# Kernel tuning notes

Hardware: AMD Instinct MI355X
Metric: run time of the kernel (lower is better)

Reference implementation:

```python
import jax, jax.numpy as jnp
import numpy as np

H = 768        # hidden_size (rubert-base)
WDIM = 30      # width_embedding_dim (SpanRepresentation default)
MAXW = 10      # max_span_width
HID = 150      # PairwiseScorer hidden_dim
LN_EPS = 1e-5


def setup_inputs() -> dict:
    key = jax.random.key(0)
    ks = jax.random.split(key, 12)
    B, S, N = 4, 2048, 4096
    p = lambda i, shape: jax.random.normal(ks[i], shape, dtype=jnp.float32) * 0.02
    return {
        "sequence_output": jax.random.normal(ks[0], (B, S, H), dtype=jnp.float32),
        "span_starts": jax.random.randint(ks[1], (B, N), 0, S),
        "span_ends": jax.random.randint(ks[2], (B, N), 0, S),
        "W_start": p(3, (H, H)), "b_start": jnp.zeros((H,), jnp.float32),
        "W_end": p(4, (H, H)), "b_end": jnp.zeros((H,), jnp.float32),
        "width_emb": p(5, (MAXW + 1, WDIM)),
        "W_out": p(6, (2 * H + WDIM, H)), "b_out": jnp.zeros((H,), jnp.float32),
        "w_ment": p(7, (H,)), "b_ment": jnp.zeros((), jnp.float32),
        "W1": p(8, (4 * H, HID)), "b1": jnp.zeros((HID,), jnp.float32),
        "ln_g": jnp.ones((HID,), jnp.float32), "ln_b": jnp.zeros((HID,), jnp.float32),
        "W2": p(9, (HID,)), "b2": jnp.zeros((), jnp.float32),
        "top_k": 128,
    }


def reference(sequence_output, span_starts, span_ends,
              W_start, b_start, W_end, b_end, width_emb, W_out, b_out,
              w_ment, b_ment, W1, b1, ln_g, ln_b, W2, b2, top_k):
    # --- SpanRepresentation: gather endpoints, endpoint FFs, width embedding ---
    st = jnp.take_along_axis(sequence_output, span_starts[..., None], axis=1)  # [B,N,H]
    en = jnp.take_along_axis(sequence_output, span_ends[..., None], axis=1)    # [B,N,H]
    start_e = st @ W_start + b_start
    end_e = en @ W_end + b_end
    widths = jnp.clip(span_ends - span_starts, 0, MAXW)
    we = width_emb[widths]                                                     # [B,N,WDIM]
    span_repr = jnp.concatenate([start_e, end_e, we], axis=-1) @ W_out + b_out # [B,N,H]

    # --- MentionScorer + top-k filtering (per batch, vectorized) ---
    scores = span_repr @ w_ment + b_ment                                       # [B,N]
    mention_scores, idx = jax.lax.top_k(scores, top_k)                         # [B,K]
    repr_k = jnp.take_along_axis(span_repr, idx[..., None], axis=1)            # [B,K,H]
    f_starts = jnp.take_along_axis(span_starts, idx, axis=1)
    f_ends = jnp.take_along_axis(span_ends, idx, axis=1)

    # --- PairwiseScorer over all pairs: cat([s1,s2,s1-s2,s1*s2]) @ W1 ---
    # Split W1 rows into the four feature blocks; fold the (s1-s2) block in:
    #   z = s1@(Wa+Wc) + s2@(Wb-Wc) + (s1*s2)@Wd + b1
    Wa, Wb, Wc, Wd = W1[:H], W1[H:2*H], W1[2*H:3*H], W1[3*H:]
    u = repr_k @ (Wa + Wc)                                                     # [B,K,HID]
    v = repr_k @ (Wb - Wc)                                                     # [B,K,HID]
    pw = jnp.einsum('bih,bjh,hd->bijd', repr_k, repr_k, Wd)                    # [B,K,K,HID]
    z = u[:, :, None, :] + v[:, None, :, :] + pw + b1
    h = jax.nn.relu(z)
    mu = jnp.mean(h, axis=-1, keepdims=True)
    var = jnp.mean(jnp.square(h - mu), axis=-1, keepdims=True)
    hn = (h - mu) * jax.lax.rsqrt(var + LN_EPS) * ln_g + ln_b
    # Dropout(0.3) is identity in eval mode.
    ant = hn @ W2 + b2                                                         # [B,K,K]
    ant = jnp.tril(ant, k=-1)

    return (mention_scores, ant, f_starts, f_ends)
```

## Files before the change

kernel.cpp:

```cpp
#include <hip/hip_runtime.h>
#include <math.h>

#define H 768
#define SEQ 2048
#define NSP 4096
#define HIDD 150
#define TOPK 128
#define NPAD 160

#define OFS_ANT 512
#define OFS_FS 66048
#define OFS_FE 66560

static const size_t OFF_T     = 0ull;
static const size_t OFF_BIASP = 8448ull;
static const size_t OFF_WOV   = 14592ull;
static const size_t OFF_AV    = 16128ull;
static const size_t OFF_CV    = 16896ull;
static const size_t OFF_TW    = 17664ull;
static const size_t OFF_PD    = 17680ull;
static const size_t OFF_CAND  = 34064ull;
static const size_t OFF_FS    = 42256ull;
static const size_t OFF_FE    = 42768ull;
static const size_t OFF_WID   = 43280ull;
static const size_t OFF_UVP   = 43792ull;
static const size_t OFF_GW    = 371472ull;
static const size_t OFF_SCAL  = 371632ull;
static const size_t OFF_WF    = 371640ull;
static const size_t OFF_WCF   = 433080ull;
static const size_t OFF_RJF   = 555960ull;
static const size_t OFF_RKH   = 752568ull;
static const size_t OFF_SE    = 949176ull;
static const size_t OFF_SEP   = 1735608ull;

typedef __attribute__((ext_vector_type(8))) _Float16 half8;
typedef __attribute__((ext_vector_type(4))) float f32x4;

__global__ __launch_bounds__(256) void kA(
    const float* __restrict__ b_start, const float* __restrict__ b_end,
    const float* __restrict__ b_out, const float* __restrict__ W_out,
    const float* __restrict__ w_ment, const float* __restrict__ W1,
    const float* __restrict__ ln_g, const float* __restrict__ ln_b,
    const float* __restrict__ W2, const float* __restrict__ b2,
    float* __restrict__ biasP, float* __restrict__ WOV,
    _Float16* __restrict__ WF, _Float16* __restrict__ WCF,
    float* __restrict__ GW, float* __restrict__ SCAL) {
    const int blk = blockIdx.x, tid = threadIdx.x;
    if (blk < 24) {
        const int kc = blk / 3, jb = blk - kc * 3;
        const int j = jb * 256 + tid;
        float acc = (kc == 0) ? b_out[j] : 0.f;
        const int k0 = kc * 96;
#pragma unroll 4
        for (int k = k0; k < k0 + 96; ++k) {
            acc += b_start[k] * W_out[(size_t)k * H + j];
            acc += b_end[k]   * W_out[(size_t)(H + k) * H + j];
        }
        biasP[kc * H + j] = acc;
    } else if (blk < 408) {
        const int wid = tid >> 6, lane = tid & 63;
        const int gr = (blk - 24) * 4 + wid;
        const float* row = W_out + (size_t)gr * H;
        float s = 0.f;
#pragma unroll
        for (int q = 0; q < 12; ++q) s += row[lane + 64 * q] * w_ment[lane + 64 * q];
#pragma unroll
        for (int off = 32; off; off >>= 1) s += __shfl_down(s, off, 64);
        if (lane == 0) WOV[gr] = s;
    } else if (blk < 468) {
        const int idx = (blk - 408) * 256 + tid;
        const int nt = idx / 1536;
        const int rem = idx - nt * 1536;
        const int kt = rem >> 6, lane = rem & 63;
        const int n = nt * 16 + (lane & 15);
        const int kb = kt * 32 + (lane >> 4) * 8;
        _Float16* dst = WF + (size_t)idx * 8;
#pragma unroll
        for (int e = 0; e < 8; ++e) {
            float v = (n < HIDD) ? W1[(size_t)(3 * H + kb + e) * HIDD + n] : 0.f;
            dst[e] = (_Float16)v;
        }
    } else if (blk < 588) {
        const int idx = (blk - 468) * 256 + tid;
        const int nt = idx / 1536;
        const int rem = idx - nt * 1536;
        const int kt = rem >> 6, lane = rem & 63;
        const int n = nt * 16 + (lane & 15);
        const int kb = kt * 32 + (lane >> 4) * 8;
        _Float16* dst = WCF + (size_t)idx * 8;
#pragma unroll
        for (int e = 0; e < 8; ++e) {
            const int h = kb + e;
            float v = 0.f;
            if (n < 160) {
                if (n < HIDD)
                    v = W1[(size_t)h * HIDD + n] + W1[(size_t)(2 * H + h) * HIDD + n];
            } else {
                const int d = n - 160;
                if (d < HIDD)
                    v = W1[(size_t)(H + h) * HIDD + d] - W1[(size_t)(2 * H + h) * HIDD + d];
            }
            dst[e] = (_Float16)v;
        }
    } else {
        if (tid < NPAD) GW[tid] = (tid < HIDD) ? ln_g[tid] * W2[tid] : 0.f;
        if (tid == 0) {
            float sg = 0.f, sb = 0.f;
            for (int d = 0; d < HIDD; ++d) { sg += ln_g[d] * W2[d]; sb += ln_b[d] * W2[d]; }
            SCAL[0] = sg;
            SCAL[1] = sb + b2[0];
        }
    }
}

__global__ __launch_bounds__(256) void kB(
    const float* __restrict__ biasP, const float* __restrict__ width_emb,
    const float* __restrict__ W_out, const float* __restrict__ W_start,
    const float* __restrict__ W_end, const float* __restrict__ WOV,
    float* __restrict__ T, float* __restrict__ av, float* __restrict__ cv) {
    const int blk = blockIdx.x, tid = threadIdx.x;
    if (blk < 33) {
        const int w = blk / 3, jb = blk - w * 3;
        const int j = jb * 256 + tid;
        float acc = 0.f;
#pragma unroll
        for (int kc = 0; kc < 8; ++kc) acc += biasP[kc * H + j];
#pragma unroll
        for (int k = 0; k < 30; ++k)
            acc += width_emb[w * 30 + k] * W_out[(size_t)(2 * H + k) * H + j];
        T[w * H + j] = acc;
    } else {
        const int wid = tid >> 6, lane = tid & 63;
        const int gr = (blk - 33) * 4 + wid;
        const float* row = (gr < H) ? (W_start + (size_t)gr * H) : (W_end + (size_t)(gr - H) * H);
        const float* vec = (gr < H) ? WOV : (WOV + H);
        float s = 0.f;
#pragma unroll
        for (int q = 0; q < 12; ++q) s += row[lane + 64 * q] * vec[lane + 64 * q];
#pragma unroll
        for (int off = 32; off; off >>= 1) s += __shfl_down(s, off, 64);
        if (lane == 0) {
            if (gr < H) av[gr] = s; else cv[gr - H] = s;
        }
    }
}

__global__ void k_posdots(const float* __restrict__ seq, const float* __restrict__ av,
                          const float* __restrict__ cv, const float* __restrict__ T,
                          const float* __restrict__ w_ment, const float* __restrict__ b_ment,
                          float* __restrict__ PD, float* __restrict__ tw) {
    const int wid = threadIdx.x >> 6, lane = threadIdx.x & 63;
    if (blockIdx.x < 2048) {
        const int r = blockIdx.x * 4 + wid;
        const float4* row = (const float4*)(seq + (size_t)r * H);
        const float4* a4 = (const float4*)av;
        const float4* c4 = (const float4*)cv;
        float sa = 0.f, sc = 0.f;
#pragma unroll
        for (int q = 0; q < 3; ++q) {
            float4 x = row[lane + 64 * q];
            float4 ya = a4[lane + 64 * q], yc = c4[lane + 64 * q];
            sa += x.x * ya.x + x.y * ya.y + x.z * ya.z + x.w * ya.w;
            sc += x.x * yc.x + x.y * yc.y + x.z * yc.z + x.w * yc.w;
        }
#pragma unroll
        for (int off = 32; off; off >>= 1) {
            sa += __shfl_down(sa, off, 64);
            sc += __shfl_down(sc, off, 64);
        }
        if (lane == 0) { PD[r] = sa; PD[8192 + r] = sc; }
    } else {
        for (int w = wid; w <= 10; w += 4) {
            float s = 0.f;
#pragma unroll
            for (int q = 0; q < 12; ++q) s += T[w * H + lane + 64 * q] * w_ment[lane + 64 * q];
#pragma unroll
            for (int off = 32; off; off >>= 1) s += __shfl_down(s, off, 64);
            if (lane == 0) tw[w] = s + b_ment[0];
        }
    }
}

__global__ __launch_bounds__(256) void k_sort1(const float* __restrict__ PD,
    const int* __restrict__ starts, const int* __restrict__ ends,
    const float* __restrict__ tw, unsigned long long* __restrict__ CAND) {
    __shared__ unsigned long long keys[512];
    const int blk = blockIdx.x;
    const int b = blk >> 3, c = blk & 7;
    const int tid = threadIdx.x;
    for (int i = tid; i < 512; i += 256) {
        const int gi = c * 512 + i;
        const int r = b * NSP + gi;
        const int s = starts[r], e = ends[r];
        int w = e - s; w = w < 0 ? 0 : (w > 10 ? 10 : w);
        const float sc = PD[b * SEQ + s] + PD[8192 + b * SEQ + e] + tw[w];
        unsigned u = __float_as_uint(sc);
        u = (u & 0x80000000u) ? ~u : (u | 0x80000000u);
        keys[i] = ((unsigned long long)u << 32) | (unsigned)(0xFFFFFFFFu - (unsigned)gi);
    }
    __syncthreads();
    for (int k = 2; k <= 512; k <<= 1) {
        for (int j = k >> 1; j > 0; j >>= 1) {
            const int p = tid;
            const int i = ((p & ~(j - 1)) << 1) | (p & (j - 1));
            const int l = i | j;
            unsigned long long a = keys[i], d = keys[l];
            const bool desc = ((i & k) == 0);
            if ((a < d) == desc) { keys[i] = d; keys[l] = a; }
            __syncthreads();
        }
    }
    if (tid < 128) CAND[(size_t)(b * 8 + c) * 128 + tid] = keys[tid];
}

__global__ __launch_bounds__(512) void k_sort2(const unsigned long long* __restrict__ CAND,
    const int* __restrict__ starts, const int* __restrict__ ends,
    float* __restrict__ out, int* __restrict__ fsI, int* __restrict__ feI,
    int* __restrict__ widI) {
    __shared__ unsigned long long keys[1024];
    const int b = blockIdx.x;
    const int tid = threadIdx.x;
    for (int i = tid; i < 1024; i += 512) keys[i] = CAND[(size_t)b * 1024 + i];
    __syncthreads();
    for (int k = 2; k <= 1024; k <<= 1) {
        for (int j = k >> 1; j > 0; j >>= 1) {
            const int p = tid;
            const int i = ((p & ~(j - 1)) << 1) | (p & (j - 1));
            const int l = i | j;
            unsigned long long a = keys[i], d = keys[l];
            const bool desc = ((i & k) == 0);
            if ((a < d) == desc) { keys[i] = d; keys[l] = a; }
            __syncthreads();
        }
    }
    if (tid < TOPK) {
        const unsigned long long key = keys[tid];
        const int widx = (int)(0xFFFFFFFFu - (unsigned)(key & 0xFFFFFFFFu));
        const unsigned hu = (unsigned)(key >> 32);
        const float sval = __uint_as_float((hu & 0x80000000u) ? (hu & 0x7FFFFFFFu) : ~hu);
        const int s = starts[b * NSP + widx], e = ends[b * NSP + widx];
        const int p = b * TOPK + tid;
        out[p] = sval;
        out[OFS_FS + p] = (float)s;
        out[OFS_FE + p] = (float)e;
        fsI[p] = b * SEQ + s;
        feI[p] = b * SEQ + e;
        int w = e - s;
        widI[p] = w < 0 ? 0 : (w > 10 ? 10 : w);
    }
}

__global__ __launch_bounds__(256) void k_se(const float* __restrict__ seq,
    const int* __restrict__ fsI, const int* __restrict__ feI,
    const float* __restrict__ W_start, const float* __restrict__ W_end,
    float* __restrict__ SEP) {
    __shared__ float sA[16][68];
    __shared__ float sB[16][68];
    __shared__ int sRow[64];
    const int tid = threadIdx.x;
    const int n0 = blockIdx.x * 64, m0 = blockIdx.y * 64, z = blockIdx.z;
    const int which = z >> 2;
    const int kbase = (z & 3) * 192;
    const int* rsrc = which ? feI : fsI;
    if (tid < 64) sRow[tid] = rsrc[m0 + tid];
    __syncthreads();
    const float* W = which ? W_end : W_start;
    const int tr = tid >> 4, tc = tid & 15;
    const int rr = tid >> 2, kg = (tid & 3) * 4;
    const int kb = tid >> 4, jc = (tid & 15) * 4;
    float acc[4][4];
#pragma unroll
    for (int i = 0; i < 4; ++i)
#pragma unroll
        for (int j = 0; j < 4; ++j) acc[i][j] = 0.f;
    for (int k0 = kbase; k0 < kbase + 192; k0 += 16) {
        float4 va = *(const float4*)(seq + (size_t)sRow[rr] * H + k0 + kg);
        float4 vb = *(const float4*)(W + (size_t)(k0 + kb) * H + n0 + jc);
        sA[kg + 0][rr] = va.x; sA[kg + 1][rr] = va.y;
        sA[kg + 2][rr] = va.z; sA[kg + 3][rr] = va.w;
        *(float4*)&sB[kb][jc] = vb;
        __syncthreads();
#pragma unroll
        for (int kk = 0; kk < 16; ++kk) {
            float a[4], b[4];
            *(float4*)a = *(const float4*)&sA[kk][tr * 4];
            *(float4*)b = *(const float4*)&sB[kk][tc * 4];
#pragma unroll
            for (int i = 0; i < 4; ++i)
#pragma unroll
                for (int j = 0; j < 4; ++j) acc[i][j] += a[i] * b[j];
        }
        __syncthreads();
    }
    float* dst = SEP + (size_t)z * 512 * H;
#pragma unroll
    for (int i = 0; i < 4; ++i) {
        float4 o = make_float4(acc[i][0], acc[i][1], acc[i][2], acc[i][3]);
        *(float4*)(dst + (size_t)(m0 + tr * 4 + i) * H + n0 + tc * 4) = o;
    }
}

__global__ void k_reduceSE(const float* __restrict__ SEP, float* __restrict__ SE) {
    const int p = blockIdx.x, tid = threadIdx.x;
    if (tid >= 192) return;
    const int which = p >> 9, row = p & 511;
    const int c0 = tid * 4;
    float4 s = make_float4(0.f, 0.f, 0.f, 0.f);
#pragma unroll
    for (int kc = 0; kc < 4; ++kc) {
        float4 v = *(const float4*)(SEP + ((size_t)((which << 2) | kc) * 512 + row) * H + c0);
        s.x += v.x; s.y += v.y; s.z += v.z; s.w += v.w;
    }
    *(float4*)(SE + (size_t)p * H + c0) = s;
}

__global__ __launch_bounds__(256) void k_rk(const float* __restrict__ SE,
    const float* __restrict__ W_out, float* __restrict__ RKP) {
    __shared__ float sA[16][68];
    __shared__ float sB[16][68];
    const int tid = threadIdx.x;
    const int n0 = blockIdx.x * 64, m0 = blockIdx.y * 64, z = blockIdx.z;
    const int ph = z >> 2;
    const int kbase = (z & 3) * 192;
    const float* A = SE + (size_t)ph * 512 * H;
    const float* B = W_out + (size_t)ph * H * H;
    const int tr = tid >> 4, tc = tid & 15;
    const int rr = tid >> 2, kg = (tid & 3) * 4;
    const int kb = tid >> 4, jc = (tid & 15) * 4;
    float acc[4][4];
#pragma unroll
    for (int i = 0; i < 4; ++i)
#pragma unroll
        for (int j = 0; j < 4; ++j) acc[i][j] = 0.f;
    for (int k0 = kbase; k0 < kbase + 192; k0 += 16) {
        float4 va = *(const float4*)(A + (size_t)(m0 + rr) * H + k0 + kg);
        float4 vb = *(const float4*)(B + (size_t)(k0 + kb) * H + n0 + jc);
        sA[kg + 0][rr] = va.x; sA[kg + 1][rr] = va.y;
        sA[kg + 2][rr] = va.z; sA[kg + 3][rr] = va.w;
        *(float4*)&sB[kb][jc] = vb;
        __syncthreads();
#pragma unroll
        for (int kk = 0; kk < 16; ++kk) {
            float a[4], b[4];
            *(float4*)a = *(const float4*)&sA[kk][tr * 4];
            *(float4*)b = *(const float4*)&sB[kk][tc * 4];
#pragma unroll
            for (int i = 0; i < 4; ++i)
#pragma unroll
                for (int j = 0; j < 4; ++j) acc[i][j] += a[i] * b[j];
        }
        __syncthreads();
    }
    float* dst = RKP + (size_t)z * 512 * H;
#pragma unroll
    for (int i = 0; i < 4; ++i) {
        float4 o = make_float4(acc[i][0], acc[i][1], acc[i][2], acc[i][3]);
        *(float4*)(dst + (size_t)(m0 + tr * 4 + i) * H + n0 + tc * 4) = o;
    }
}

__global__ __launch_bounds__(256) void k_reduce(const float* __restrict__ RKpart,
    const float* __restrict__ T, const int* __restrict__ widI,
    _Float16* __restrict__ RKH, _Float16* __restrict__ RJF) {
    __shared__ float srow[H];
    const int p = blockIdx.x, tid = threadIdx.x;
    const int w = widI[p];
    if (tid < 192) {
        const int c0 = tid * 4;
        float4 s = *(const float4*)(T + (size_t)w * H + c0);
#pragma unroll
        for (int kc = 0; kc < 8; ++kc) {
            float4 v = *(const float4*)(RKpart + ((size_t)kc * 512 + p) * H + c0);
            s.x += v.x; s.y += v.y; s.z += v.z; s.w += v.w;
        }
        *(float4*)&srow[c0] = s;
        _Float16* hd = RKH + (size_t)p * H + c0;
        hd[0] = (_Float16)s.x; hd[1] = (_Float16)s.y;
        hd[2] = (_Float16)s.z; hd[3] = (_Float16)s.w;
    }
    __syncthreads();
    if (tid < 96) {
        const int k0 = tid * 8;
        const int kt = k0 >> 5, sub = k0 & 31;
        const int lane = (p & 15) | ((sub >> 3) << 4);
        const int t = p >> 4;
        _Float16* d2 = RJF + ((size_t)(t * 24 + kt) * 64 + lane) * 8;
#pragma unroll
        for (int e = 0; e < 8; ++e) d2[e] = (_Float16)srow[k0 + e];
    }
}

__global__ __launch_bounds__(256) void k_uv3(const _Float16* __restrict__ RJF,
    const _Float16* __restrict__ WCF, float* __restrict__ UVP) {
    const int t = blockIdx.x, kh = blockIdx.y;
    const int wave = threadIdx.x >> 6, lane = threadIdx.x & 63;
    const _Float16* Af = RJF + (size_t)t * 24 * 64 * 8;
    f32x4 acc[5];
#pragma unroll
    for (int q = 0; q < 5; ++q) acc[q] = (f32x4){0.f, 0.f, 0.f, 0.f};
    for (int kk = 0; kk < 12; ++kk) {
        const int kt = kh * 12 + kk;
        half8 a = *(const half8*)(Af + ((size_t)(kt * 64 + lane)) * 8);
#pragma unroll
        for (int q = 0; q < 5; ++q) {
            const int nt = wave * 5 + q;
            half8 bv = *(const half8*)(WCF + ((size_t)((nt * 24 + kt) * 64 + lane)) * 8);
            acc[q] = __builtin_amdgcn_mfma_f32_16x16x32_f16(a, bv, acc[q], 0, 0, 0);
        }
    }
    const int c = lane & 15, g = lane >> 4;
#pragma unroll
    for (int q = 0; q < 5; ++q) {
        const int n = (wave * 5 + q) * 16 + c;
#pragma unroll
        for (int r = 0; r < 4; ++r) {
            const int p = t * 16 + g * 4 + r;
            UVP[((size_t)kh * 512 + p) * 320 + n] = acc[q][r];
        }
    }
}

__global__ __launch_bounds__(256) void k_pair(
    const _Float16* __restrict__ RJF, const _Float16* __restrict__ WF,
    const _Float16* __restrict__ RKH, const float* __restrict__ UVP,
    const float* __restrict__ b1, const float* __restrict__ GW,
    const float* __restrict__ SCAL, float* __restrict__ ant) {
    const int ii = blockIdx.x, b = blockIdx.y;
    float* arow = ant + ((size_t)b * TOPK + ii) * TOPK;
    const int tid = threadIdx.x;
    if (tid < TOPK && tid >= ii) arow[tid] = 0.f;
    const int ntiles = (ii + 15) >> 4;
    if (ntiles == 0) return;

    const int wave = tid >> 6, lane = tid & 63;
    const int g = lane >> 4, c = lane & 15;
    const int t0 = wave, t1 = wave + 4;
    const bool has0 = t0 < ntiles, has1 = t1 < ntiles;

    __shared__ _Float16 sB[2][5120];

    const _Float16* RiH = RKH + (size_t)(b * TOPK + ii) * H;
    const _Float16* Aj0 = RJF + (size_t)(b * 8 + t0) * 24 * 64 * 8;
    const _Float16* Aj1 = RJF + (size_t)(b * 8 + (t1 < 8 ? t1 : 7)) * 24 * 64 * 8;

    f32x4 acc0[10], acc1[10];
#pragma unroll
    for (int nt = 0; nt < 10; ++nt) {
        acc0[nt] = (f32x4){0.f, 0.f, 0.f, 0.f};
        acc1[nt] = (f32x4){0.f, 0.f, 0.f, 0.f};
    }

    auto stage_src = [&](int kt, int i) -> uint4 {
        const int nt = i >> 6, wi = i & 63;
        return *(const uint4*)(WF + ((size_t)((nt * 24 + kt) * 64 + wi)) * 8);
    };

    uint4 s0 = stage_src(0, tid);
    uint4 s1 = stage_src(0, tid + 256);
    uint4 s2;
    if (tid < 128) s2 = stage_src(0, tid + 512);
    {
        uint4* sbw = (uint4*)sB[0];
        sbw[tid] = s0;
        sbw[tid + 256] = s1;
        if (tid < 128) sbw[tid + 512] = s2;
    }
    half8 rj0, rj1, ri;
    if (has0) rj0 = *(const half8*)(Aj0 + (size_t)lane * 8);
    if (has1) rj1 = *(const half8*)(Aj1 + (size_t)lane * 8);
    ri = *(const half8*)(RiH + g * 8);
    __syncthreads();

    for (int kt = 0; kt < 24; ++kt) {
        const int cur = kt & 1, nxt = cur ^ 1;
        uint4 n0, n1, n2;
        half8 nrj0, nrj1, nri;
        if (kt < 23) {
            n0 = stage_src(kt + 1, tid);
            n1 = stage_src(kt + 1, tid + 256);
            if (tid < 128) n2 = stage_src(kt + 1, tid + 512);
            if (has0) nrj0 = *(const half8*)(Aj0 + ((size_t)((kt + 1) * 64 + lane)) * 8);
            if (has1) nrj1 = *(const half8*)(Aj1 + ((size_t)((kt + 1) * 64 + lane)) * 8);
            nri = *(const half8*)(RiH + (kt + 1) * 32 + g * 8);
        }
        half8 a0, a1;
        if (has0) a0 = ri * rj0;
        if (has1) a1 = ri * rj1;
#pragma unroll
        for (int nt = 0; nt < 10; ++nt) {
            half8 bv = *(const half8*)&sB[cur][nt * 512 + lane * 8];
            if (has0) acc0[nt] = __builtin_amdgcn_mfma_f32_16x16x32_f16(a0, bv, acc0[nt], 0, 0, 0);
            if (has1) acc1[nt] = __builtin_amdgcn_mfma_f32_16x16x32_f16(a1, bv, acc1[nt], 0, 0, 0);
        }
        if (kt < 23) {
            uint4* sbw = (uint4*)sB[nxt];
            sbw[tid] = n0;
            sbw[tid + 256] = n1;
            if (tid < 128) sbw[tid + 512] = n2;
            rj0 = nrj0; rj1 = nrj1; ri = nri;
        }
        __syncthreads();
    }

    const float Sgw = SCAL[0], C0 = SCAL[1];
    const int pi = b * TOPK + ii;
    float u10[10], gw10[10];
#pragma unroll
    for (int nt = 0; nt < 10; ++nt) {
        const int d = nt * 16 + c;
        const float ub = (d < HIDD) ? b1[d] : 0.f;
        u10[nt] = UVP[(size_t)pi * 320 + d] + UVP[(size_t)(512 + pi) * 320 + d] + ub;
        gw10[nt] = GW[d];
    }
    auto epi = [&](const f32x4 (&acc)[10], int t) {
#pragma unroll
        for (int r = 0; r < 4; ++r) {
            const int j = 16 * t + g * 4 + r;
            const int pj = b * TOPK + j;
            const float* Vp0 = UVP + (size_t)pj * 320 + 160;
            const float* Vp1 = UVP + (size_t)(512 + pj) * 320 + 160;
            float s1 = 0.f, s2 = 0.f, s3 = 0.f;
#pragma unroll
            for (int nt = 0; nt < 10; ++nt) {
                const int d = nt * 16 + c;
                float z = acc[nt][r] + u10[nt] + Vp0[d] + Vp1[d];
                float h = (d < HIDD && z > 0.f) ? z : 0.f;
                s1 += h;
                s2 += h * h;
                s3 += h * gw10[nt];
            }
#pragma unroll
            for (int off = 1; off < 16; off <<= 1) {
                s1 += __shfl_xor(s1, off, 64);
                s2 += __shfl_xor(s2, off, 64);
                s3 += __shfl_xor(s3, off, 64);
            }
            const float mu = s1 * (1.f / HIDD);
            const float var = s2 * (1.f / HIDD) - mu * mu;
            const float rstd = rsqrtf(var + 1e-5f);
            const float val = rstd * (s3 - mu * Sgw) + C0;
            if (c == 0 && j < ii) arow[j] = val;
        }
    };
    if (has0) epi(acc0, t0);
    if (has1) epi(acc1, t1);
}

extern "C" void kernel_launch(void* const* d_in, const int* in_sizes, int n_in,
                              void* d_out, int out_size, void* d_ws, size_t ws_size,
                              hipStream_t stream) {
    const float* seq      = (const float*)d_in[0];
    const int*   starts   = (const int*)d_in[1];
    const int*   ends     = (const int*)d_in[2];
    const float* W_start  = (const float*)d_in[3];
    const float* b_start  = (const float*)d_in[4];
    const float* W_end    = (const float*)d_in[5];
    const float* b_end    = (const float*)d_in[6];
    const float* width_e  = (const float*)d_in[7];
    const float* W_out    = (const float*)d_in[8];
    const float* b_out    = (const float*)d_in[9];
    const float* w_ment   = (const float*)d_in[10];
    const float* b_ment   = (const float*)d_in[11];
    const float* W1       = (const float*)d_in[12];
    const float* b1       = (const float*)d_in[13];
    const float* ln_g     = (const float*)d_in[14];
    const float* ln_b     = (const float*)d_in[15];
    const float* W2       = (const float*)d_in[16];
    const float* b2       = (const float*)d_in[17];
    float* out = (float*)d_out;
    float* ws  = (float*)d_ws;

    float* Tt    = ws + OFF_T;
    float* biasP = ws + OFF_BIASP;
    float* WOV   = ws + OFF_WOV;
    float* av    = ws + OFF_AV;
    float* cv    = ws + OFF_CV;
    float* tw    = ws + OFF_TW;
    float* PD    = ws + OFF_PD;
    unsigned long long* CANDp = (unsigned long long*)(ws + OFF_CAND);
    int*   fsI   = (int*)(ws + OFF_FS);
    int*   feI   = (int*)(ws + OFF_FE);
    int*   widI  = (int*)(ws + OFF_WID);
    float* UVPp  = ws + OFF_UVP;
    float* GWp   = ws + OFF_GW;
    float* SCALp = ws + OFF_SCAL;
    _Float16* WFp  = (_Float16*)(ws + OFF_WF);
    _Float16* WCFp = (_Float16*)(ws + OFF_WCF);
    _Float16* RJFp = (_Float16*)(ws + OFF_RJF);
    _Float16* RKHp = (_Float16*)(ws + OFF_RKH);
    float* SEp   = ws + OFF_SE;
    float* SEPp  = ws + OFF_SEP;

    kA<<<589, 256, 0, stream>>>(b_start, b_end, b_out, W_out, w_ment, W1,
                                ln_g, ln_b, W2, b2, biasP, WOV, WFp, WCFp, GWp, SCALp);
    kB<<<417, 256, 0, stream>>>(biasP, width_e, W_out, W_start, W_end, WOV, Tt, av, cv);
    k_posdots<<<2049, 256, 0, stream>>>(seq, av, cv, Tt, w_ment, b_ment, PD, tw);
    k_sort1<<<32, 256, 0, stream>>>(PD, starts, ends, tw, CANDp);
    k_sort2<<<4, 512, 0, stream>>>(CANDp, starts, ends, out, fsI, feI, widI);
    k_se<<<dim3(12, 8, 8), 256, 0, stream>>>(seq, fsI, feI, W_start, W_end, SEPp);
    k_reduceSE<<<1024, 192, 0, stream>>>(SEPp, SEp);
    k_rk<<<dim3(12, 8, 8), 256, 0, stream>>>(SEp, W_out, SEPp);
    k_reduce<<<512, 256, 0, stream>>>(SEPp, Tt, widI, RKHp, RJFp);
    k_uv3<<<dim3(32, 2), 256, 0, stream>>>(RJFp, WCFp, UVPp);
    k_pair<<<dim3(128, 4), 256, 0, stream>>>(RJFp, WFp, RKHp, UVPp, b1, GWp, SCALp,
                                             out + OFS_ANT);
}
```

Baseline: 237.5 us.

## Move top-k span projection GEMMs to fp16 MFMA and replace final bitonic sort with merge

```diff
diff --git a/kernel.cpp b/kernel.cpp
--- a/kernel.cpp
+++ b/kernel.cpp
@@ -28,12 +28,16 @@
 static const size_t OFF_SCAL  = 371632ull;
 static const size_t OFF_WF    = 371640ull;
 static const size_t OFF_WCF   = 433080ull;
-static const size_t OFF_RJF   = 555960ull;
-static const size_t OFF_RKH   = 752568ull;
-static const size_t OFF_SE    = 949176ull;
-static const size_t OFF_SEP   = 1735608ull;
+static const size_t OFF_WSF   = 555960ull;
+static const size_t OFF_WEF   = 850872ull;
+static const size_t OFF_WOF   = 1145784ull;
+static const size_t OFF_GSEH  = 1735608ull;
+static const size_t OFF_SEH   = 2128824ull;
+static const size_t OFF_RKH   = 2522040ull;
+static const size_t OFF_RKP2  = 2718648ull;
 
 typedef __attribute__((ext_vector_type(8))) _Float16 half8;
+typedef __attribute__((ext_vector_type(4))) _Float16 half4;
 typedef __attribute__((ext_vector_type(4))) float f32x4;
 
 __global__ __launch_bounds__(256) void kA(
@@ -42,9 +46,11 @@
     const float* __restrict__ w_ment, const float* __restrict__ W1,
     const float* __restrict__ ln_g, const float* __restrict__ ln_b,
     const float* __restrict__ W2, const float* __restrict__ b2,
+    const float* __restrict__ W_start, const float* __restrict__ W_end,
     float* __restrict__ biasP, float* __restrict__ WOV,
     _Float16* __restrict__ WF, _Float16* __restrict__ WCF,
-    float* __restrict__ GW, float* __restrict__ SCAL) {
+    _Float16* __restrict__ WSF, _Float16* __restrict__ WEF,
+    _Float16* __restrict__ WOF, float* __restrict__ GW, float* __restrict__ SCAL) {
     const int blk = blockIdx.x, tid = threadIdx.x;
     if (blk < 24) {
         const int kc = blk / 3, jb = blk - kc * 3;
@@ -102,7 +108,7 @@
             }
             dst[e] = (_Float16)v;
         }
-    } else {
+    } else if (blk == 588) {
         if (tid < NPAD) GW[tid] = (tid < HIDD) ? ln_g[tid] * W2[tid] : 0.f;
         if (tid == 0) {
             float sg = 0.f, sb = 0.f;
@@ -110,6 +116,29 @@
             SCAL[0] = sg;
             SCAL[1] = sb + b2[0];
         }
+    } else if (blk < 1165) {
+        const bool isS = blk < 877;
+        const int idx = (blk - (isS ? 589 : 877)) * 256 + tid;
+        const float* Wsrc = isS ? W_start : W_end;
+        _Float16* dstb = isS ? WSF : WEF;
+        const int nt = idx / 1536;
+        const int rem = idx - nt * 1536;
+        const int kt = rem >> 6, lane = rem & 63;
+        const int n = nt * 16 + (lane & 15);
+        const int kb = kt * 32 + (lane >> 4) * 8;
+        _Float16* dst = dstb + (size_t)idx * 8;
+#pragma unroll
+        for (int e = 0; e < 8; ++e) dst[e] = (_Float16)Wsrc[(size_t)(kb + e) * H + n];
+    } else {
+        const int idx = (blk - 1165) * 256 + tid;
+        const int nt = idx / 3072;
+        const int rem = idx - nt * 3072;
+        const int kt = rem >> 6, lane = rem & 63;
+        const int n = nt * 16 + (lane & 15);
+        const int kb = kt * 32 + (lane >> 4) * 8;
+        _Float16* dst = WOF + (size_t)idx * 8;
+#pragma unroll
+        for (int e = 0; e < 8; ++e) dst[e] = (_Float16)W_out[(size_t)(kb + e) * H + n];
     }
 }
 
@@ -213,28 +242,48 @@
     if (tid < 128) CAND[(size_t)(b * 8 + c) * 128 + tid] = keys[tid];
 }
 
-__global__ __launch_bounds__(512) void k_sort2(const unsigned long long* __restrict__ CAND,
+__global__ __launch_bounds__(256) void k_sort2(const unsigned long long* __restrict__ CAND,
     const int* __restrict__ starts, const int* __restrict__ ends,
     float* __restrict__ out, int* __restrict__ fsI, int* __restrict__ feI,
     int* __restrict__ widI) {
-    __shared__ unsigned long long keys[1024];
-    const int b = blockIdx.x;
-    const int tid = threadIdx.x;
-    for (int i = tid; i < 1024; i += 512) keys[i] = CAND[(size_t)b * 1024 + i];
+    __shared__ unsigned long long K[1024];
+    const int b = blockIdx.x, tid = threadIdx.x;
+    for (int i = tid; i < 1024; i += 256) K[i] = CAND[(size_t)b * 1024 + i];
     __syncthreads();
-    for (int k = 2; k <= 1024; k <<= 1) {
-        for (int j = k >> 1; j > 0; j >>= 1) {
-            const int p = tid;
-            const int i = ((p & ~(j - 1)) << 1) | (p & (j - 1));
-            const int l = i | j;
-            unsigned long long a = keys[i], d = keys[l];
-            const bool desc = ((i & k) == 0);
-            if ((a < d) == desc) { keys[i] = d; keys[l] = a; }
+    for (int nl = 4; nl >= 1; nl >>= 1) {
+        const int items = nl * 128;
+        unsigned long long v0 = 0, v1 = 0;
+        if (tid < items) {
+            const int q = tid >> 7, r = tid & 127;
+            unsigned long long a = K[q * 256 + r];
+            unsigned long long d = K[q * 256 + 128 + (127 - r)];
+            v0 = a > d ? a : d;
+        }
+        if (tid + 256 < items) {
+            const int i = tid + 256;
+            const int q = i >> 7, r = i & 127;
+            unsigned long long a = K[q * 256 + r];
+            unsigned long long d = K[q * 256 + 128 + (127 - r)];
+            v1 = a > d ? a : d;
+        }
+        __syncthreads();
+        if (tid < items) K[(tid >> 7) * 128 + (tid & 127)] = v0;
+        if (tid + 256 < items) { const int i = tid + 256; K[(i >> 7) * 128 + (i & 127)] = v1; }
+        __syncthreads();
+        for (int j = 64; j; j >>= 1) {
+            const int pairs = nl * 64;
+            for (int i = tid; i < pairs; i += 256) {
+                const int q = i >> 6, r = i & 63;
+                const int lo = q * 128 + (((r & ~(j - 1)) << 1) | (r & (j - 1)));
+                const int hi = lo + j;
+                unsigned long long a = K[lo], d = K[hi];
+                if (a < d) { K[lo] = d; K[hi] = a; }
+            }
             __syncthreads();
         }
     }
     if (tid < TOPK) {
-        const unsigned long long key = keys[tid];
+        const unsigned long long key = K[tid];
         const int widx = (int)(0xFFFFFFFFu - (unsigned)(key & 0xFFFFFFFFu));
         const unsigned hu = (unsigned)(key >> 32);
         const float sval = __uint_as_float((hu & 0x80000000u) ? (hu & 0x7FFFFFFFu) : ~hu);
@@ -250,157 +299,96 @@
     }
 }
 
-__global__ __launch_bounds__(256) void k_se(const float* __restrict__ seq,
-    const int* __restrict__ fsI, const int* __restrict__ feI,
-    const float* __restrict__ W_start, const float* __restrict__ W_end,
-    float* __restrict__ SEP) {
-    __shared__ float sA[16][68];
-    __shared__ float sB[16][68];
-    __shared__ int sRow[64];
+__global__ void k_gath(const float* __restrict__ seq, const int* __restrict__ fsI,
+                       const int* __restrict__ feI, _Float16* __restrict__ GSEH) {
+    const int r0 = blockIdx.x * 4;
     const int tid = threadIdx.x;
-    const int n0 = blockIdx.x * 64, m0 = blockIdx.y * 64, z = blockIdx.z;
-    const int which = z >> 2;
-    const int kbase = (z & 3) * 192;
-    const int* rsrc = which ? feI : fsI;
-    if (tid < 64) sRow[tid] = rsrc[m0 + tid];
-    __syncthreads();
-    const float* W = which ? W_end : W_start;
-    const int tr = tid >> 4, tc = tid & 15;
-    const int rr = tid >> 2, kg = (tid & 3) * 4;
-    const int kb = tid >> 4, jc = (tid & 15) * 4;
-    float acc[4][4];
-#pragma unroll
-    for (int i = 0; i < 4; ++i)
-#pragma unroll
-        for (int j = 0; j < 4; ++j) acc[i][j] = 0.f;
-    for (int k0 = kbase; k0 < kbase + 192; k0 += 16) {
-        float4 va = *(const float4*)(seq + (size_t)sRow[rr] * H + k0 + kg);
-        float4 vb = *(const float4*)(W + (size_t)(k0 + kb) * H + n0 + jc);
-        sA[kg + 0][rr] = va.x; sA[kg + 1][rr] = va.y;
-        sA[kg + 2][rr] = va.z; sA[kg + 3][rr] = va.w;
-        *(float4*)&sB[kb][jc] = vb;
-        __syncthreads();
-#pragma unroll
-        for (int kk = 0; kk < 16; ++kk) {
-            float a[4], b[4];
-            *(float4*)a = *(const float4*)&sA[kk][tr * 4];
-            *(float4*)b = *(const float4*)&sB[kk][tc * 4];
-#pragma unroll
-            for (int i = 0; i < 4; ++i)
-#pragma unroll
-                for (int j = 0; j < 4; ++j) acc[i][j] += a[i] * b[j];
-        }
-        __syncthreads();
-    }
-    float* dst = SEP + (size_t)z * 512 * H;
-#pragma unroll
-    for (int i = 0; i < 4; ++i) {
-        float4 o = make_float4(acc[i][0], acc[i][1], acc[i][2], acc[i][3]);
-        *(float4*)(dst + (size_t)(m0 + tr * 4 + i) * H + n0 + tc * 4) = o;
-    }
-}
-
-__global__ void k_reduceSE(const float* __restrict__ SEP, float* __restrict__ SE) {
+    for (int q = 0; q < 4; ++q) {
+        const int row = r0 + q;
+        const int src = (row < 512) ? fsI[row] : feI[row - 512];
+        if (tid < 192) {
+            float4 v = *(const float4*)(seq + (size_t)src * H + tid * 4);
+            half4 h = {(_Float16)v.x, (_Float16)v.y, (_Float16)v.z, (_Float16)v.w};
+            *(half4*)(GSEH + (size_t)row * H + tid * 4) = h;
+        }
+    }
+}
+
+__global__ __launch_bounds__(256) void k_gemm1(const _Float16* __restrict__ GSEH,
+    const _Float16* __restrict__ WSF, const _Float16* __restrict__ WEF,
+    _Float16* __restrict__ SEH) {
+    const int mt = blockIdx.x;
+    const int wave = threadIdx.x >> 6, lane = threadIdx.x & 63;
+    const int nt0 = blockIdx.y * 8 + wave * 2;
+    const _Float16* Arow = GSEH + (size_t)(mt * 16 + (lane & 15)) * H + (lane >> 4) * 8;
+    const _Float16* BF = (mt < 32) ? WSF : WEF;
+    f32x4 acc0 = {0.f, 0.f, 0.f, 0.f}, acc1 = acc0;
+    for (int kt = 0; kt < 24; ++kt) {
+        half8 a = *(const half8*)(Arow + kt * 32);
+        half8 b0 = *(const half8*)(BF + ((size_t)((nt0 * 24 + kt) * 64 + lane)) * 8);
+        half8 b1 = *(const half8*)(BF + ((size_t)(((nt0 + 1) * 24 + kt) * 64 + lane)) * 8);
+        acc0 = __builtin_amdgcn_mfma_f32_16x16x32_f16(a, b0, acc0, 0, 0, 0);
+        acc1 = __builtin_amdgcn_mfma_f32_16x16x32_f16(a, b1, acc1, 0, 0, 0);
+    }
+    const int c = lane & 15, quad = lane >> 4;
+#pragma unroll
+    for (int r = 0; r < 4; ++r) {
+        const int row = mt * 16 + quad * 4 + r;
+        SEH[(size_t)row * H + nt0 * 16 + c] = (_Float16)acc0[r];
+        SEH[(size_t)row * H + (nt0 + 1) * 16 + c] = (_Float16)acc1[r];
+    }
+}
+
+__global__ __launch_bounds__(256) void k_gemm2(const _Float16* __restrict__ SEH,
+    const _Float16* __restrict__ WOF, float* __restrict__ RKP2) {
+    const int mt = blockIdx.x, kh = blockIdx.z;
+    const int wave = threadIdx.x >> 6, lane = threadIdx.x & 63;
+    const int nt0 = blockIdx.y * 8 + wave * 2;
+    const _Float16* Arow = SEH + (size_t)(kh * 512 + mt * 16 + (lane & 15)) * H + (lane >> 4) * 8;
+    f32x4 acc0 = {0.f, 0.f, 0.f, 0.f}, acc1 = acc0;
+    for (int kt2 = 0; kt2 < 24; ++kt2) {
+        const int kt = kh * 24 + kt2;
+        half8 a = *(const half8*)(Arow + kt2 * 32);
+        half8 b0 = *(const half8*)(WOF + ((size_t)((nt0 * 48 + kt) * 64 + lane)) * 8);
+        half8 b1 = *(const half8*)(WOF + ((size_t)(((nt0 + 1) * 48 + kt) * 64 + lane)) * 8);
+        acc0 = __builtin_amdgcn_mfma_f32_16x16x32_f16(a, b0, acc0, 0, 0, 0);
+        acc1 = __builtin_amdgcn_mfma_f32_16x16x32_f16(a, b1, acc1, 0, 0, 0);
+    }
+    const int c = lane & 15, quad = lane >> 4;
+    float* dst = RKP2 + (size_t)kh * 512 * H;
+#pragma unroll
+    for (int r = 0; r < 4; ++r) {
+        const int row = mt * 16 + quad * 4 + r;
+        dst[(size_t)row * H + nt0 * 16 + c] = acc0[r];
+        dst[(size_t)row * H + (nt0 + 1) * 16 + c] = acc1[r];
+    }
+}
+
+__global__ void k_fin(const float* __restrict__ RKP2, const float* __restrict__ T,
+                      const int* __restrict__ widI, _Float16* __restrict__ RKH) {
     const int p = blockIdx.x, tid = threadIdx.x;
     if (tid >= 192) return;
-    const int which = p >> 9, row = p & 511;
+    const int w = widI[p];
     const int c0 = tid * 4;
-    float4 s = make_float4(0.f, 0.f, 0.f, 0.f);
-#pragma unroll
-    for (int kc = 0; kc < 4; ++kc) {
-        float4 v = *(const float4*)(SEP + ((size_t)((which << 2) | kc) * 512 + row) * H + c0);
-        s.x += v.x; s.y += v.y; s.z += v.z; s.w += v.w;
-    }
-    *(float4*)(SE + (size_t)p * H + c0) = s;
-}
-
-__global__ __launch_bounds__(256) void k_rk(const float* __restrict__ SE,
-    const float* __restrict__ W_out, float* __restrict__ RKP) {
-    __shared__ float sA[16][68];
-    __shared__ float sB[16][68];
-    const int tid = threadIdx.x;
-    const int n0 = blockIdx.x * 64, m0 = blockIdx.y * 64, z = blockIdx.z;
-    const int ph = z >> 2;
-    const int kbase = (z & 3) * 192;
-    const float* A = SE + (size_t)ph * 512 * H;
-    const float* B = W_out + (size_t)ph * H * H;
-    const int tr = tid >> 4, tc = tid & 15;
-    const int rr = tid >> 2, kg = (tid & 3) * 4;
-    const int kb = tid >> 4, jc = (tid & 15) * 4;
-    float acc[4][4];
-#pragma unroll
-    for (int i = 0; i < 4; ++i)
-#pragma unroll
-        for (int j = 0; j < 4; ++j) acc[i][j] = 0.f;
-    for (int k0 = kbase; k0 < kbase + 192; k0 += 16) {
-        float4 va = *(const float4*)(A + (size_t)(m0 + rr) * H + k0 + kg);
-        float4 vb = *(const float4*)(B + (size_t)(k0 + kb) * H + n0 + jc);
-        sA[kg + 0][rr] = va.x; sA[kg + 1][rr] = va.y;
-        sA[kg + 2][rr] = va.z; sA[kg + 3][rr] = va.w;
-        *(float4*)&sB[kb][jc] = vb;
-        __syncthreads();
-#pragma unroll
-        for (int kk = 0; kk < 16; ++kk) {
-            float a[4], b[4];
-            *(float4*)a = *(const float4*)&sA[kk][tr * 4];
-            *(float4*)b = *(const float4*)&sB[kk][tc * 4];
-#pragma unroll
-            for (int i = 0; i < 4; ++i)
-#pragma unroll
-                for (int j = 0; j < 4; ++j) acc[i][j] += a[i] * b[j];
-        }
-        __syncthreads();
-    }
-    float* dst = RKP + (size_t)z * 512 * H;
-#pragma unroll
-    for (int i = 0; i < 4; ++i) {
-        float4 o = make_float4(acc[i][0], acc[i][1], acc[i][2], acc[i][3]);
-        *(float4*)(dst + (size_t)(m0 + tr * 4 + i) * H + n0 + tc * 4) = o;
-    }
-}
-
-__global__ __launch_bounds__(256) void k_reduce(const float* __restrict__ RKpart,
-    const float* __restrict__ T, const int* __restrict__ widI,
-    _Float16* __restrict__ RKH, _Float16* __restrict__ RJF) {
-    __shared__ float srow[H];
-    const int p = blockIdx.x, tid = threadIdx.x;
-    const int w = widI[p];
-    if (tid < 192) {
-        const int c0 = tid * 4;
-        float4 s = *(const float4*)(T + (size_t)w * H + c0);
-#pragma unroll
-        for (int kc = 0; kc < 8; ++kc) {
-            float4 v = *(const float4*)(RKpart + ((size_t)kc * 512 + p) * H + c0);
-            s.x += v.x; s.y += v.y; s.z += v.z; s.w += v.w;
-        }
-        *(float4*)&srow[c0] = s;
-        _Float16* hd = RKH + (size_t)p * H + c0;
-        hd[0] = (_Float16)s.x; hd[1] = (_Float16)s.y;
-        hd[2] = (_Float16)s.z; hd[3] = (_Float16)s.w;
-    }
-    __syncthreads();
-    if (tid < 96) {
-        const int k0 = tid * 8;
-        const int kt = k0 >> 5, sub = k0 & 31;
-        const int lane = (p & 15) | ((sub >> 3) << 4);
-        const int t = p >> 4;
-        _Float16* d2 = RJF + ((size_t)(t * 24 + kt) * 64 + lane) * 8;
-#pragma unroll
-        for (int e = 0; e < 8; ++e) d2[e] = (_Float16)srow[k0 + e];
-    }
-}
-
-__global__ __launch_bounds__(256) void k_uv3(const _Float16* __restrict__ RJF,
+    float4 s = *(const float4*)(T + (size_t)w * H + c0);
+    float4 v0 = *(const float4*)(RKP2 + (size_t)p * H + c0);
+    float4 v1 = *(const float4*)(RKP2 + (size_t)(512 + p) * H + c0);
+    half4 h = {(_Float16)(s.x + v0.x + v1.x), (_Float16)(s.y + v0.y + v1.y),
+               (_Float16)(s.z + v0.z + v1.z), (_Float16)(s.w + v0.w + v1.w)};
+    *(half4*)(RKH + (size_t)p * H + c0) = h;
+}
+
+__global__ __launch_bounds__(256) void k_uv3(const _Float16* __restrict__ RKH,
     const _Float16* __restrict__ WCF, float* __restrict__ UVP) {
     const int t = blockIdx.x, kh = blockIdx.y;
     const int wave = threadIdx.x >> 6, lane = threadIdx.x & 63;
-    const _Float16* Af = RJF + (size_t)t * 24 * 64 * 8;
+    const _Float16* Arow = RKH + (size_t)(t * 16 + (lane & 15)) * H + (lane >> 4) * 8;
     f32x4 acc[5];
 #pragma unroll
     for (int q = 0; q < 5; ++q) acc[q] = (f32x4){0.f, 0.f, 0.f, 0.f};
     for (int kk = 0; kk < 12; ++kk) {
         const int kt = kh * 12 + kk;
-        half8 a = *(const half8*)(Af + ((size_t)(kt * 64 + lane)) * 8);
+        half8 a = *(const half8*)(Arow + kt * 32);
 #pragma unroll
         for (int q = 0; q < 5; ++q) {
             const int nt = wave * 5 + q;
@@ -421,10 +409,10 @@
 }
 
 __global__ __launch_bounds__(256) void k_pair(
-    const _Float16* __restrict__ RJF, const _Float16* __restrict__ WF,
-    const _Float16* __restrict__ RKH, const float* __restrict__ UVP,
-    const float* __restrict__ b1, const float* __restrict__ GW,
-    const float* __restrict__ SCAL, float* __restrict__ ant) {
+    const _Float16* __restrict__ WF, const _Float16* __restrict__ RKH,
+    const float* __restrict__ UVP, const float* __restrict__ b1,
+    const float* __restrict__ GW, const float* __restrict__ SCAL,
+    float* __restrict__ ant) {
     const int ii = blockIdx.x, b = blockIdx.y;
     float* arow = ant + ((size_t)b * TOPK + ii) * TOPK;
     const int tid = threadIdx.x;
@@ -440,8 +428,8 @@
     __shared__ _Float16 sB[2][5120];
 
     const _Float16* RiH = RKH + (size_t)(b * TOPK + ii) * H;
-    const _Float16* Aj0 = RJF + (size_t)(b * 8 + t0) * 24 * 64 * 8;
-    const _Float16* Aj1 = RJF + (size_t)(b * 8 + (t1 < 8 ? t1 : 7)) * 24 * 64 * 8;
+    const _Float16* Rj0 = RKH + (size_t)(b * TOPK + t0 * 16 + c) * H + g * 8;
+    const _Float16* Rj1 = RKH + (size_t)(b * TOPK + t1 * 16 + c) * H + g * 8;
 
     f32x4 acc0[10], acc1[10];
 #pragma unroll
@@ -466,8 +454,8 @@
         if (tid < 128) sbw[tid + 512] = s2;
     }
     half8 rj0, rj1, ri;
-    if (has0) rj0 = *(const half8*)(Aj0 + (size_t)lane * 8);
-    if (has1) rj1 = *(const half8*)(Aj1 + (size_t)lane * 8);
+    if (has0) rj0 = *(const half8*)(Rj0);
+    if (has1) rj1 = *(const half8*)(Rj1);
     ri = *(const half8*)(RiH + g * 8);
     __syncthreads();
 
@@ -479,8 +467,8 @@
             n0 = stage_src(kt + 1, tid);
             n1 = stage_src(kt + 1, tid + 256);
             if (tid < 128) n2 = stage_src(kt + 1, tid + 512);
-            if (has0) nrj0 = *(const half8*)(Aj0 + ((size_t)((kt + 1) * 64 + lane)) * 8);
-            if (has1) nrj1 = *(const half8*)(Aj1 + ((size_t)((kt + 1) * 64 + lane)) * 8);
+            if (has0) nrj0 = *(const half8*)(Rj0 + (kt + 1) * 32);
+            if (has1) nrj1 = *(const half8*)(Rj1 + (kt + 1) * 32);
             nri = *(const half8*)(RiH + (kt + 1) * 32 + g * 8);
         }
         half8 a0, a1;
@@ -584,24 +572,28 @@
     float* UVPp  = ws + OFF_UVP;
     float* GWp   = ws + OFF_GW;
     float* SCALp = ws + OFF_SCAL;
-    _Float16* WFp  = (_Float16*)(ws + OFF_WF);
-    _Float16* WCFp = (_Float16*)(ws + OFF_WCF);
-    _Float16* RJFp = (_Float16*)(ws + OFF_RJF);
-    _Float16* RKHp = (_Float16*)(ws + OFF_RKH);
-    float* SEp   = ws + OFF_SE;
-    float* SEPp  = ws + OFF_SEP;
-
-    kA<<<589, 256, 0, stream>>>(b_start, b_end, b_out, W_out, w_ment, W1,
-                                ln_g, ln_b, W2, b2, biasP, WOV, WFp, WCFp, GWp, SCALp);
+    _Float16* WFp   = (_Float16*)(ws + OFF_WF);
+    _Float16* WCFp  = (_Float16*)(ws + OFF_WCF);
+    _Float16* WSFp  = (_Float16*)(ws + OFF_WSF);
+    _Float16* WEFp  = (_Float16*)(ws + OFF_WEF);
+    _Float16* WOFp  = (_Float16*)(ws + OFF_WOF);
+    _Float16* GSEHp = (_Float16*)(ws + OFF_GSEH);
+    _Float16* SEHp  = (_Float16*)(ws + OFF_SEH);
+    _Float16* RKHp  = (_Float16*)(ws + OFF_RKH);
+    float* RKP2p = ws + OFF_RKP2;
+
+    kA<<<1741, 256, 0, stream>>>(b_start, b_end, b_out, W_out, w_ment, W1,
+                                 ln_g, ln_b, W2, b2, W_start, W_end,
+                                 biasP, WOV, WFp, WCFp, WSFp, WEFp, WOFp, GWp, SCALp);
     kB<<<417, 256, 0, stream>>>(biasP, width_e, W_out, W_start, W_end, WOV, Tt, av, cv);
     k_posdots<<<2049, 256, 0, stream>>>(seq, av, cv, Tt, w_ment, b_ment, PD, tw);
     k_sort1<<<32, 256, 0, stream>>>(PD, starts, ends, tw, CANDp);
-    k_sort2<<<4, 512, 0, stream>>>(CANDp, starts, ends, out, fsI, feI, widI);
-    k_se<<<dim3(12, 8, 8), 256, 0, stream>>>(seq, fsI, feI, W_start, W_end, SEPp);
-    k_reduceSE<<<1024, 192, 0, stream>>>(SEPp, SEp);
-    k_rk<<<dim3(12, 8, 8), 256, 0, stream>>>(SEp, W_out, SEPp);
-    k_reduce<<<512, 256, 0, stream>>>(SEPp, Tt, widI, RKHp, RJFp);
-    k_uv3<<<dim3(32, 2), 256, 0, stream>>>(RJFp, WCFp, UVPp);
-    k_pair<<<dim3(128, 4), 256, 0, stream>>>(RJFp, WFp, RKHp, UVPp, b1, GWp, SCALp,
+    k_sort2<<<4, 256, 0, stream>>>(CANDp, starts, ends, out, fsI, feI, widI);
+    k_gath<<<256, 256, 0, stream>>>(seq, fsI, feI, GSEHp);
+    k_gemm1<<<dim3(64, 6), 256, 0, stream>>>(GSEHp, WSFp, WEFp, SEHp);
+    k_gemm2<<<dim3(32, 6, 2), 256, 0, stream>>>(SEHp, WOFp, RKP2p);
+    k_fin<<<512, 192, 0, stream>>>(RKP2p, Tt, widI, RKHp);
+    k_uv3<<<dim3(32, 2), 256, 0, stream>>>(RKHp, WCFp, UVPp);
+    k_pair<<<dim3(128, 4), 256, 0, stream>>>(WFp, RKHp, UVPp, b1, GWp, SCALp,
                                              out + OFS_ANT);
 }
```

Result: faster. 210.3 us (-11.5%).
